# Kernel optimization log

Hardware: AMD Instinct MI355X
Metric: run time of the kernel (lower is better)

## Reference

```python
import jax, jax.numpy as jnp
import numpy as np

N_NODES = 100000


def gcn_conv(x, edge_index, W, b, num_nodes):
    """PyG GCNConv: y = D^{-1/2} (A + I) D^{-1/2} (x W) + b.

    edge_index[0] = source (row), edge_index[1] = target (col);
    messages flow source -> target with symmetric normalization.
    """
    # add self loops
    loop = jnp.arange(num_nodes, dtype=edge_index.dtype)
    row = jnp.concatenate([edge_index[0], loop])  # [E+N]
    col = jnp.concatenate([edge_index[1], loop])  # [E+N]

    xw = x @ W  # [N, F_out] -- tiny GEMM, done before gather

    # degree of target nodes (incl. self loops)
    ones = jnp.ones(col.shape[0], dtype=x.dtype)
    deg = jax.ops.segment_sum(ones, col, num_segments=num_nodes)  # [N]
    dis = jax.lax.rsqrt(jnp.maximum(deg, 1e-12))
    dis = jnp.where(deg > 0, dis, 0.0)

    norm = dis[row] * dis[col]  # [E+N]
    msg = xw[row] * norm[:, None]  # gather + scale, [E+N, F_out]
    out = jax.ops.segment_sum(msg, col, num_segments=num_nodes)  # scatter-add
    return out + b


def setup_inputs() -> dict:
    key = jax.random.key(0)
    k1, k2, k3, k4 = jax.random.split(key, 4)
    num_attr, hidden, num_classes = 128, 16, 8
    n_edges = 3200000
    x = jax.random.normal(k1, (N_NODES, num_attr), dtype=jnp.float32)
    edge_index = jax.random.randint(k2, (2, n_edges), 0, N_NODES, dtype=jnp.int64)
    W1 = jax.random.normal(k3, (num_attr, hidden), dtype=jnp.float32) / np.sqrt(num_attr)
    b1 = jnp.zeros((hidden,), dtype=jnp.float32)
    W2 = jax.random.normal(k4, (hidden, num_classes), dtype=jnp.float32) / np.sqrt(hidden)
    b2 = jnp.zeros((num_classes,), dtype=jnp.float32)
    return {"x": x, "edge_index": edge_index, "W1": W1, "b1": b1, "W2": W2, "b2": b2}


def reference(x, edge_index, W1, b1, W2, b2):
    h = gcn_conv(x, edge_index, W1, b1, N_NODES)
    h = jax.nn.relu(h)
    # dropout is identity in eval mode
    h = gcn_conv(h, edge_index, W2, b2, N_NODES)
    return jax.nn.sigmoid(h)  # [N, num_classes]
```

## Files before the change

### kernel.cpp

```cpp
#include <hip/hip_runtime.h>
#include <math.h>

static constexpr int FI = 128;
static constexpr int FH = 16;
static constexpr int FO = 8;

static constexpr int BIN_SHIFT = 8;
static constexpr int BIN_NODES = 256;
static constexpr int MAX_BINS  = 512;
static constexpr int CAPB      = 8832;
static constexpr int SCHUNK    = 8192;
static constexpr int SThreads  = 512;

__device__ __forceinline__ unsigned short f2bf(float x) {
    unsigned u = __float_as_uint(x);
    u += 0x7FFFu + ((u >> 16) & 1u);
    return (unsigned short)(u >> 16);
}
__device__ __forceinline__ float bflo(unsigned u) { return __uint_as_float(u << 16); }
__device__ __forceinline__ float bfhi(unsigned u) { return __uint_as_float(u & 0xFFFF0000u); }

__global__ void k_initcur(int* __restrict__ binCursor, int nbins) {
    int i = blockIdx.x * 256 + threadIdx.x;
    if (i < nbins) binCursor[i] = i * CAPB;
}

__launch_bounds__(SThreads)
__global__ void k_binscatter(const int* __restrict__ row, const int* __restrict__ col,
                             int* __restrict__ binCursor, unsigned int* __restrict__ binned,
                             int E, int nbins) {
    __shared__ int lcnt[MAX_BINS];
    __shared__ int lsc[MAX_BINS];
    __shared__ int lstart[MAX_BINS];
    __shared__ int lcur[MAX_BINS];
    __shared__ int gbase[MAX_BINS];
    __shared__ unsigned int   staged[SCHUNK];
    __shared__ unsigned short sbin[SCHUNK];
    int t = threadIdx.x;
    int base = blockIdx.x * SCHUNK;
    int end  = base + SCHUNK; if (end > E) end = E;
    int m = end - base;
    if (t < MAX_BINS) lcnt[t] = 0;
    __syncthreads();

    int nv = m >> 2;
    const int4* c4 = (const int4*)(col + base);
    int4 creg[4];
    #pragma unroll
    for (int j = 0; j < 4; ++j) {
        int k = t + j * SThreads;
        if (k < nv) {
            creg[j] = c4[k];
            atomicAdd(&lcnt[creg[j].x >> BIN_SHIFT], 1);
            atomicAdd(&lcnt[creg[j].y >> BIN_SHIFT], 1);
            atomicAdd(&lcnt[creg[j].z >> BIN_SHIFT], 1);
            atomicAdd(&lcnt[creg[j].w >> BIN_SHIFT], 1);
        }
    }
    for (int i = base + (nv << 2) + t; i < end; i += SThreads)
        atomicAdd(&lcnt[col[i] >> BIN_SHIFT], 1);
    __syncthreads();

    int v = 0;
    if (t < MAX_BINS) { v = lcnt[t]; lsc[t] = v; }
    __syncthreads();
    for (int off = 1; off < MAX_BINS; off <<= 1) {
        int x = (t >= off && t < MAX_BINS) ? lsc[t - off] : 0;
        __syncthreads();
        if (t < MAX_BINS) lsc[t] += x;
        __syncthreads();
    }
    if (t < MAX_BINS) {
        int ex = lsc[t] - v;
        lstart[t] = ex;
        lcur[t]   = ex;
        gbase[t]  = v ? atomicAdd(&binCursor[t], v) : 0;
    }
    __syncthreads();

    const int4* r4 = (const int4*)(row + base);
    #pragma unroll
    for (int j = 0; j < 4; ++j) {
        int k = t + j * SThreads;
        if (k < nv) {
            int4 r = r4[k];
            int cc[4] = {creg[j].x, creg[j].y, creg[j].z, creg[j].w};
            int rr[4] = {r.x, r.y, r.z, r.w};
            #pragma unroll
            for (int jj = 0; jj < 4; ++jj) {
                int b = cc[jj] >> BIN_SHIFT;
                int pos = atomicAdd(&lcur[b], 1);
                staged[pos] = (unsigned)rr[jj] | ((unsigned)(cc[jj] & (BIN_NODES - 1)) << 17);
                sbin[pos] = (unsigned short)b;
            }
        }
    }
    for (int i = base + (nv << 2) + t; i < end; i += SThreads) {
        int c = col[i];
        int b = c >> BIN_SHIFT;
        int pos = atomicAdd(&lcur[b], 1);
        staged[pos] = (unsigned)row[i] | ((unsigned)(c & (BIN_NODES - 1)) << 17);
        sbin[pos] = (unsigned short)b;
    }
    __syncthreads();

    for (int i = t; i < m; i += SThreads) {
        int b = sbin[i];
        int g = gbase[b] + (i - lstart[b]);
        if (g < (b + 1) * CAPB) binned[g] = staged[i];
    }
}

__launch_bounds__(256)
__global__ void k_refine_gemm(const int* __restrict__ binCursor, const unsigned int* __restrict__ binned,
                              int* __restrict__ srow, int* __restrict__ starts, int* __restrict__ ends,
                              float* __restrict__ dis, const float* __restrict__ x,
                              const float* __restrict__ W1, unsigned short* __restrict__ xw1s, int N) {
    __shared__ int cnt[BIN_NODES];
    __shared__ int wsum[4];
    __shared__ float sdis[BIN_NODES];
    __shared__ float sw[FI * FH];
    __shared__ float sx[64 * 132];
    int t = threadIdx.x;
    int b = blockIdx.x;
    int s = b * CAPB;
    int m = binCursor[b] - s;
    if (m > CAPB) m = CAPB;
    cnt[t] = 0;
    for (int i = t; i < FI * FH; i += 256) sw[i] = W1[i];
    __syncthreads();

    int mm = m & ~3;
    for (int i0 = t * 4; i0 < mm; i0 += BIN_NODES * 4) {
        uint4 v = *(const uint4*)(binned + s + i0);
        atomicAdd(&cnt[v.x >> 17], 1);
        atomicAdd(&cnt[v.y >> 17], 1);
        atomicAdd(&cnt[v.z >> 17], 1);
        atomicAdd(&cnt[v.w >> 17], 1);
    }
    for (int i = mm + t; i < m; i += BIN_NODES)
        atomicAdd(&cnt[binned[s + i] >> 17], 1);
    __syncthreads();

    int deg = cnt[t];
    int inc = deg;
    #pragma unroll
    for (int d = 1; d < 64; d <<= 1) {
        int u = __shfl_up(inc, d, 64);
        if ((t & 63) >= d) inc += u;
    }
    if ((t & 63) == 63) wsum[t >> 6] = inc;
    __syncthreads();
    if (t < 4) {
        int w = wsum[t];
        #pragma unroll
        for (int d = 1; d < 4; d <<= 1) {
            int u = __shfl_up(w, d, 4);
            if (t >= d) w += u;
        }
        wsum[t] = w;
    }
    __syncthreads();
    int waveoff = (t >= 64) ? wsum[(t >> 6) - 1] : 0;
    int excl = waveoff + inc - deg;

    int n = b * BIN_NODES + t;
    float dv = rsqrtf((float)(deg + 1));
    if (n < N) {
        starts[n] = s + excl;
        ends[n]   = s + excl + deg;
        dis[n]    = dv;
    }
    sdis[t] = dv;
    cnt[t] = excl;
    __syncthreads();

    for (int i0 = t * 4; i0 < mm; i0 += BIN_NODES * 4) {
        uint4 v = *(const uint4*)(binned + s + i0);
        int p0 = atomicAdd(&cnt[v.x >> 17], 1); srow[s + p0] = v.x & 0x1FFFF;
        int p1 = atomicAdd(&cnt[v.y >> 17], 1); srow[s + p1] = v.y & 0x1FFFF;
        int p2 = atomicAdd(&cnt[v.z >> 17], 1); srow[s + p2] = v.z & 0x1FFFF;
        int p3 = atomicAdd(&cnt[v.w >> 17], 1); srow[s + p3] = v.w & 0x1FFFF;
    }
    for (int i = mm + t; i < m; i += BIN_NODES) {
        unsigned v = binned[s + i];
        int p = atomicAdd(&cnt[v >> 17], 1);
        srow[s + p] = v & 0x1FFFF;
    }

    int nl = t >> 2;
    int f  = (t & 3) * 4;
    for (int c = 0; c < 4; ++c) {
        __syncthreads();
        int rbase = b * BIN_NODES + c * 64;
        int rows = N - rbase;
        rows = rows < 0 ? 0 : (rows > 64 ? 64 : rows);
        const float4* xg = (const float4*)(x + (size_t)rbase * FI);
        for (int i = t; i < rows * 32; i += 256) {
            int r = i >> 5, cc = i & 31;
            float4 vv = xg[(size_t)r * 32 + cc];
            float* dst = &sx[r * 132 + cc * 4];
            dst[0] = vv.x; dst[1] = vv.y; dst[2] = vv.z; dst[3] = vv.w;
        }
        __syncthreads();
        int nn = rbase + nl;
        if (nn < N) {
            float a0 = 0.f, a1 = 0.f, a2 = 0.f, a3 = 0.f;
            #pragma unroll 4
            for (int k = 0; k < FI; k++) {
                float xv = sx[nl * 132 + k];
                const float* wr = &sw[k * FH + f];
                a0 = fmaf(xv, wr[0], a0);
                a1 = fmaf(xv, wr[1], a1);
                a2 = fmaf(xv, wr[2], a2);
                a3 = fmaf(xv, wr[3], a3);
            }
            float dn = sdis[c * 64 + nl];
            unsigned w0 = (unsigned)f2bf(a0 * dn) | ((unsigned)f2bf(a1 * dn) << 16);
            unsigned w1 = (unsigned)f2bf(a2 * dn) | ((unsigned)f2bf(a3 * dn) << 16);
            *(uint2*)(xw1s + (size_t)nn * FH + f) = make_uint2(w0, w1);
        }
    }
}

__launch_bounds__(256)
__global__ void k_agg1(const int* __restrict__ starts, const int* __restrict__ ends,
                       const int* __restrict__ srow, const float* __restrict__ dis,
                       const unsigned short* __restrict__ xw1s, const float* __restrict__ W2,
                       const float* __restrict__ b1, unsigned short* __restrict__ xw2s, int N) {
    __shared__ float sw[FH * FO];
    __shared__ float sb[FH];
    int t = threadIdx.x;
    if (t < FH * FO) sw[t] = W2[t];
    if (t < FH) sb[t] = b1[t];
    __syncthreads();

    int n = blockIdx.x * 128 + (t >> 1);
    int h = t & 1;
    if (n >= N) return;
    float dn = dis[n];
    int s = starts[n], e = ends[n];
    const uint4* xq = (const uint4*)xw1s;

    uint4 sp = xq[(size_t)n * 2 + h];
    float acc[8];
    acc[0]=bflo(sp.x); acc[1]=bfhi(sp.x); acc[2]=bflo(sp.y); acc[3]=bfhi(sp.y);
    acc[4]=bflo(sp.z); acc[5]=bfhi(sp.z); acc[6]=bflo(sp.w); acc[7]=bfhi(sp.w);

    int i = s;
    for (; i + 8 <= e; i += 8) {
        int rr[8];
        #pragma unroll
        for (int j = 0; j < 8; ++j) rr[j] = srow[i + j];
        uint4 pk[8];
        #pragma unroll
        for (int j = 0; j < 8; ++j) pk[j] = xq[(size_t)rr[j] * 2 + h];
        #pragma unroll
        for (int j = 0; j < 8; ++j) {
            acc[0]+=bflo(pk[j].x); acc[1]+=bfhi(pk[j].x);
            acc[2]+=bflo(pk[j].y); acc[3]+=bfhi(pk[j].y);
            acc[4]+=bflo(pk[j].z); acc[5]+=bfhi(pk[j].z);
            acc[6]+=bflo(pk[j].w); acc[7]+=bfhi(pk[j].w);
        }
    }
    for (; i < e; ++i) {
        uint4 p = xq[(size_t)srow[i] * 2 + h];
        acc[0]+=bflo(p.x); acc[1]+=bfhi(p.x);
        acc[2]+=bflo(p.y); acc[3]+=bfhi(p.y);
        acc[4]+=bflo(p.z); acc[5]+=bfhi(p.z);
        acc[6]+=bflo(p.w); acc[7]+=bfhi(p.w);
    }

    float hv[8];
    #pragma unroll
    for (int k = 0; k < 8; ++k) {
        float v = fmaf(dn, acc[k], sb[h * 8 + k]);
        hv[k] = v > 0.f ? v : 0.f;
    }
    float po[FO];
    #pragma unroll
    for (int o = 0; o < FO; ++o) {
        float a = 0.f;
        #pragma unroll
        for (int k = 0; k < 8; ++k) a = fmaf(hv[k], sw[(h * 8 + k) * FO + o], a);
        po[o] = a;
    }
    #pragma unroll
    for (int o = 0; o < FO; ++o) po[o] += __shfl_xor(po[o], 1, 64);
    int o0 = h * 4;
    unsigned w0 = (unsigned)f2bf(po[o0 + 0] * dn) | ((unsigned)f2bf(po[o0 + 1] * dn) << 16);
    unsigned w1 = (unsigned)f2bf(po[o0 + 2] * dn) | ((unsigned)f2bf(po[o0 + 3] * dn) << 16);
    *(uint2*)(xw2s + (size_t)n * FO + o0) = make_uint2(w0, w1);
}

__launch_bounds__(256)
__global__ void k_agg2(const int* __restrict__ starts, const int* __restrict__ ends,
                       const int* __restrict__ srow, const float* __restrict__ dis,
                       const unsigned short* __restrict__ xw2s, const float* __restrict__ b2,
                       float* __restrict__ out, int N) {
    int t = threadIdx.x;
    int n = blockIdx.x * 128 + (t >> 1);
    int h = t & 1;
    if (n >= N) return;
    float dn = dis[n];
    int s = starts[n], e = ends[n];
    const uint2* xq = (const uint2*)xw2s;

    uint2 sp = xq[(size_t)n * 2 + h];
    float acc[4];
    acc[0]=bflo(sp.x); acc[1]=bfhi(sp.x); acc[2]=bflo(sp.y); acc[3]=bfhi(sp.y);

    int i = s;
    for (; i + 8 <= e; i += 8) {
        int rr[8];
        #pragma unroll
        for (int j = 0; j < 8; ++j) rr[j] = srow[i + j];
        uint2 pk[8];
        #pragma unroll
        for (int j = 0; j < 8; ++j) pk[j] = xq[(size_t)rr[j] * 2 + h];
        #pragma unroll
        for (int j = 0; j < 8; ++j) {
            acc[0]+=bflo(pk[j].x); acc[1]+=bfhi(pk[j].x);
            acc[2]+=bflo(pk[j].y); acc[3]+=bfhi(pk[j].y);
        }
    }
    for (; i < e; ++i) {
        uint2 p = xq[(size_t)srow[i] * 2 + h];
        acc[0]+=bflo(p.x); acc[1]+=bfhi(p.x);
        acc[2]+=bflo(p.y); acc[3]+=bfhi(p.y);
    }

    int f0 = h * 4;
    float r[4];
    #pragma unroll
    for (int k = 0; k < 4; ++k) {
        float v = fmaf(dn, acc[k], b2[f0 + k]);
        r[k] = 1.f / (1.f + __expf(-v));
    }
    *(float4*)(out + (size_t)n * FO + f0) = make_float4(r[0], r[1], r[2], r[3]);
}

extern "C" void kernel_launch(void* const* d_in, const int* in_sizes, int n_in,
                              void* d_out, int out_size, void* d_ws, size_t ws_size,
                              hipStream_t stream) {
    const float* x  = (const float*)d_in[0];
    const int*   ei = (const int*)d_in[1];
    const float* W1 = (const float*)d_in[2];
    const float* b1 = (const float*)d_in[3];
    const float* W2 = (const float*)d_in[4];
    const float* b2 = (const float*)d_in[5];

    const int N = in_sizes[0] / FI;
    const int E = in_sizes[1] / 2;
    const int* row = ei;
    const int* col = ei + E;
    const int nbins = (N + BIN_NODES - 1) >> BIN_SHIFT;

    const size_t NP = 100352;
    const size_t BINSZ = (size_t)nbins * CAPB;
    float* base = (float*)d_ws;
    int*   starts    = (int*)base;
    int*   ends      = (int*)(base + NP);
    float* dis       = base + 2 * NP;
    int*   binCursor = (int*)(base + 3 * NP);
    unsigned int* binned = (unsigned int*)(base + 3 * NP + 1024);
    int*   srow      = (int*)(base + 3 * NP + 1024 + BINSZ);
    unsigned short* xw1s = (unsigned short*)(base + 3 * NP + 1024 + 2 * BINSZ);
    unsigned short* xw2s = (unsigned short*)(base + 3 * NP + 1024 + 2 * BINSZ + NP * 8);
    float* out = (float*)d_out;

    size_t needed = (3 * NP + 1024 + 2 * BINSZ + NP * 12) * 4;
    if (ws_size < needed) return;

    k_initcur    <<<(nbins + 255) / 256, 256,             0, stream>>>(binCursor, nbins);
    k_binscatter <<<(E + SCHUNK - 1) / SCHUNK, SThreads,  0, stream>>>(row, col, binCursor, binned, E, nbins);
    k_refine_gemm<<<nbins, BIN_NODES,                     0, stream>>>(binCursor, binned, srow, starts, ends, dis, x, W1, xw1s, N);
    k_agg1       <<<(2 * N + 255) / 256, 256,             0, stream>>>(starts, ends, srow, dis, xw1s, W2, b1, xw2s, N);
    k_agg2       <<<(2 * N + 255) / 256, 256,             0, stream>>>(starts, ends, srow, dis, xw2s, b2, out, N);
}
```

Baseline: 125.9 us.

## Split refine and GEMM kernels, stage bins in LDS, use wave-shuffle scan

The fused refine+GEMM kernel is split into a counting-sort refine kernel and a standalone GEMM kernel launched over all nodes with 64 nodes per block. The refine step now stages the bin in LDS and records per-edge local ranks, so the second pass avoids rereading global memory and redoing atomics. The binscatter prefix scan is rewritten as a wave-shuffle scan, cutting the number of barriers. The cursor init kernel is replaced by a memset with relative offsets. This adds a kernel launch and a reread of dis from global memory, but the GEMM gets a full grid of parallelism rather than one block per bin.

```diff
diff --git a/kernel.cpp b/kernel.cpp
--- a/kernel.cpp
+++ b/kernel.cpp
@@ -20,27 +20,22 @@
 __device__ __forceinline__ float bflo(unsigned u) { return __uint_as_float(u << 16); }
 __device__ __forceinline__ float bfhi(unsigned u) { return __uint_as_float(u & 0xFFFF0000u); }
 
-__global__ void k_initcur(int* __restrict__ binCursor, int nbins) {
-    int i = blockIdx.x * 256 + threadIdx.x;
-    if (i < nbins) binCursor[i] = i * CAPB;
-}
-
 __launch_bounds__(SThreads)
 __global__ void k_binscatter(const int* __restrict__ row, const int* __restrict__ col,
                              int* __restrict__ binCursor, unsigned int* __restrict__ binned,
                              int E, int nbins) {
     __shared__ int lcnt[MAX_BINS];
-    __shared__ int lsc[MAX_BINS];
     __shared__ int lstart[MAX_BINS];
     __shared__ int lcur[MAX_BINS];
     __shared__ int gbase[MAX_BINS];
+    __shared__ int wsum[8];
     __shared__ unsigned int   staged[SCHUNK];
     __shared__ unsigned short sbin[SCHUNK];
     int t = threadIdx.x;
     int base = blockIdx.x * SCHUNK;
     int end  = base + SCHUNK; if (end > E) end = E;
     int m = end - base;
-    if (t < MAX_BINS) lcnt[t] = 0;
+    lcnt[t] = 0;
     __syncthreads();
 
     int nv = m >> 2;
@@ -61,17 +56,28 @@
         atomicAdd(&lcnt[col[i] >> BIN_SHIFT], 1);
     __syncthreads();
 
-    int v = 0;
-    if (t < MAX_BINS) { v = lcnt[t]; lsc[t] = v; }
-    __syncthreads();
-    for (int off = 1; off < MAX_BINS; off <<= 1) {
-        int x = (t >= off && t < MAX_BINS) ? lsc[t - off] : 0;
-        __syncthreads();
-        if (t < MAX_BINS) lsc[t] += x;
-        __syncthreads();
-    }
-    if (t < MAX_BINS) {
-        int ex = lsc[t] - v;
+    int v = lcnt[t];
+    int inc = v;
+    #pragma unroll
+    for (int d = 1; d < 64; d <<= 1) {
+        int u = __shfl_up(inc, d, 64);
+        if ((t & 63) >= d) inc += u;
+    }
+    if ((t & 63) == 63) wsum[t >> 6] = inc;
+    __syncthreads();
+    if (t < 8) {
+        int w = wsum[t];
+        #pragma unroll
+        for (int d = 1; d < 8; d <<= 1) {
+            int u = __shfl_up(w, d, 8);
+            if (t >= d) w += u;
+        }
+        wsum[t] = w;
+    }
+    __syncthreads();
+    {
+        int waveoff = (t >= 64) ? wsum[(t >> 6) - 1] : 0;
+        int ex = waveoff + inc - v;
         lstart[t] = ex;
         lcur[t]   = ex;
         gbase[t]  = v ? atomicAdd(&binCursor[t], v) : 0;
@@ -106,40 +112,41 @@
 
     for (int i = t; i < m; i += SThreads) {
         int b = sbin[i];
-        int g = gbase[b] + (i - lstart[b]);
-        if (g < (b + 1) * CAPB) binned[g] = staged[i];
-    }
-}
-
-__launch_bounds__(256)
-__global__ void k_refine_gemm(const int* __restrict__ binCursor, const unsigned int* __restrict__ binned,
-                              int* __restrict__ srow, int* __restrict__ starts, int* __restrict__ ends,
-                              float* __restrict__ dis, const float* __restrict__ x,
-                              const float* __restrict__ W1, unsigned short* __restrict__ xw1s, int N) {
+        int off = gbase[b] + (i - lstart[b]);
+        if (off < CAPB) binned[b * CAPB + off] = staged[i];
+    }
+}
+
+__launch_bounds__(BIN_NODES)
+__global__ void k_refine(const int* __restrict__ binCursor, const unsigned int* __restrict__ binned,
+                         int* __restrict__ srow, int* __restrict__ starts, int* __restrict__ ends,
+                         float* __restrict__ dis, int N) {
+    __shared__ unsigned int  stage[CAPB];
+    __shared__ unsigned char arr[CAPB];
     __shared__ int cnt[BIN_NODES];
     __shared__ int wsum[4];
-    __shared__ float sdis[BIN_NODES];
-    __shared__ float sw[FI * FH];
-    __shared__ float sx[64 * 132];
     int t = threadIdx.x;
     int b = blockIdx.x;
     int s = b * CAPB;
-    int m = binCursor[b] - s;
+    int m = binCursor[b];
     if (m > CAPB) m = CAPB;
     cnt[t] = 0;
-    for (int i = t; i < FI * FH; i += 256) sw[i] = W1[i];
     __syncthreads();
 
     int mm = m & ~3;
     for (int i0 = t * 4; i0 < mm; i0 += BIN_NODES * 4) {
         uint4 v = *(const uint4*)(binned + s + i0);
-        atomicAdd(&cnt[v.x >> 17], 1);
-        atomicAdd(&cnt[v.y >> 17], 1);
-        atomicAdd(&cnt[v.z >> 17], 1);
-        atomicAdd(&cnt[v.w >> 17], 1);
-    }
-    for (int i = mm + t; i < m; i += BIN_NODES)
-        atomicAdd(&cnt[binned[s + i] >> 17], 1);
+        *(uint4*)&stage[i0] = v;
+        arr[i0 + 0] = (unsigned char)atomicAdd(&cnt[v.x >> 17], 1);
+        arr[i0 + 1] = (unsigned char)atomicAdd(&cnt[v.y >> 17], 1);
+        arr[i0 + 2] = (unsigned char)atomicAdd(&cnt[v.z >> 17], 1);
+        arr[i0 + 3] = (unsigned char)atomicAdd(&cnt[v.w >> 17], 1);
+    }
+    for (int i = mm + t; i < m; i += BIN_NODES) {
+        unsigned v = binned[s + i];
+        stage[i] = v;
+        arr[i] = (unsigned char)atomicAdd(&cnt[v >> 17], 1);
+    }
     __syncthreads();
 
     int deg = cnt[t];
@@ -165,62 +172,63 @@
     int excl = waveoff + inc - deg;
 
     int n = b * BIN_NODES + t;
-    float dv = rsqrtf((float)(deg + 1));
     if (n < N) {
         starts[n] = s + excl;
         ends[n]   = s + excl + deg;
-        dis[n]    = dv;
-    }
-    sdis[t] = dv;
+        dis[n]    = rsqrtf((float)(deg + 1));
+    }
     cnt[t] = excl;
     __syncthreads();
 
     for (int i0 = t * 4; i0 < mm; i0 += BIN_NODES * 4) {
-        uint4 v = *(const uint4*)(binned + s + i0);
-        int p0 = atomicAdd(&cnt[v.x >> 17], 1); srow[s + p0] = v.x & 0x1FFFF;
-        int p1 = atomicAdd(&cnt[v.y >> 17], 1); srow[s + p1] = v.y & 0x1FFFF;
-        int p2 = atomicAdd(&cnt[v.z >> 17], 1); srow[s + p2] = v.z & 0x1FFFF;
-        int p3 = atomicAdd(&cnt[v.w >> 17], 1); srow[s + p3] = v.w & 0x1FFFF;
+        uint4 v = *(uint4*)&stage[i0];
+        srow[s + cnt[v.x >> 17] + arr[i0 + 0]] = v.x & 0x1FFFF;
+        srow[s + cnt[v.y >> 17] + arr[i0 + 1]] = v.y & 0x1FFFF;
+        srow[s + cnt[v.z >> 17] + arr[i0 + 2]] = v.z & 0x1FFFF;
+        srow[s + cnt[v.w >> 17] + arr[i0 + 3]] = v.w & 0x1FFFF;
     }
     for (int i = mm + t; i < m; i += BIN_NODES) {
-        unsigned v = binned[s + i];
-        int p = atomicAdd(&cnt[v >> 17], 1);
-        srow[s + p] = v & 0x1FFFF;
-    }
+        unsigned v = stage[i];
+        srow[s + cnt[v >> 17] + arr[i]] = v & 0x1FFFF;
+    }
+}
+
+__launch_bounds__(256)
+__global__ void k_gemm1(const float* __restrict__ x, const float* __restrict__ W,
+                        const float* __restrict__ dis, unsigned short* __restrict__ xw1s,
+                        int N) {
+    __shared__ float sw[FI * FH];
+    int t = threadIdx.x;
+    for (int i = t; i < FI * FH; i += 256) sw[i] = W[i];
+    __syncthreads();
 
     int nl = t >> 2;
     int f  = (t & 3) * 4;
-    for (int c = 0; c < 4; ++c) {
-        __syncthreads();
-        int rbase = b * BIN_NODES + c * 64;
-        int rows = N - rbase;
-        rows = rows < 0 ? 0 : (rows > 64 ? 64 : rows);
-        const float4* xg = (const float4*)(x + (size_t)rbase * FI);
-        for (int i = t; i < rows * 32; i += 256) {
-            int r = i >> 5, cc = i & 31;
-            float4 vv = xg[(size_t)r * 32 + cc];
-            float* dst = &sx[r * 132 + cc * 4];
-            dst[0] = vv.x; dst[1] = vv.y; dst[2] = vv.z; dst[3] = vv.w;
-        }
-        __syncthreads();
-        int nn = rbase + nl;
-        if (nn < N) {
-            float a0 = 0.f, a1 = 0.f, a2 = 0.f, a3 = 0.f;
-            #pragma unroll 4
-            for (int k = 0; k < FI; k++) {
-                float xv = sx[nl * 132 + k];
-                const float* wr = &sw[k * FH + f];
-                a0 = fmaf(xv, wr[0], a0);
-                a1 = fmaf(xv, wr[1], a1);
-                a2 = fmaf(xv, wr[2], a2);
-                a3 = fmaf(xv, wr[3], a3);
-            }
-            float dn = sdis[c * 64 + nl];
-            unsigned w0 = (unsigned)f2bf(a0 * dn) | ((unsigned)f2bf(a1 * dn) << 16);
-            unsigned w1 = (unsigned)f2bf(a2 * dn) | ((unsigned)f2bf(a3 * dn) << 16);
-            *(uint2*)(xw1s + (size_t)nn * FH + f) = make_uint2(w0, w1);
-        }
-    }
+    int n  = blockIdx.x * 64 + nl;
+    if (n >= N) return;
+
+    const float4* xr = (const float4*)(x + (size_t)n * FI);
+    float a0 = 0.f, a1 = 0.f, a2 = 0.f, a3 = 0.f;
+    #pragma unroll 8
+    for (int kq = 0; kq < FI / 4; ++kq) {
+        float4 xv = xr[kq];
+        float4 w0 = *(const float4*)&sw[(kq * 4 + 0) * FH + f];
+        float4 w1 = *(const float4*)&sw[(kq * 4 + 1) * FH + f];
+        float4 w2 = *(const float4*)&sw[(kq * 4 + 2) * FH + f];
+        float4 w3 = *(const float4*)&sw[(kq * 4 + 3) * FH + f];
+        a0 = fmaf(xv.x, w0.x, a0); a1 = fmaf(xv.x, w0.y, a1);
+        a2 = fmaf(xv.x, w0.z, a2); a3 = fmaf(xv.x, w0.w, a3);
+        a0 = fmaf(xv.y, w1.x, a0); a1 = fmaf(xv.y, w1.y, a1);
+        a2 = fmaf(xv.y, w1.z, a2); a3 = fmaf(xv.y, w1.w, a3);
+        a0 = fmaf(xv.z, w2.x, a0); a1 = fmaf(xv.z, w2.y, a1);
+        a2 = fmaf(xv.z, w2.z, a2); a3 = fmaf(xv.z, w2.w, a3);
+        a0 = fmaf(xv.w, w3.x, a0); a1 = fmaf(xv.w, w3.y, a1);
+        a2 = fmaf(xv.w, w3.z, a2); a3 = fmaf(xv.w, w3.w, a3);
+    }
+    float dn = dis[n];
+    unsigned w0 = (unsigned)f2bf(a0 * dn) | ((unsigned)f2bf(a1 * dn) << 16);
+    unsigned w1 = (unsigned)f2bf(a2 * dn) | ((unsigned)f2bf(a3 * dn) << 16);
+    *(uint2*)(xw1s + (size_t)n * FH + f) = make_uint2(w0, w1);
 }
 
 __launch_bounds__(256)
@@ -372,9 +380,10 @@
     size_t needed = (3 * NP + 1024 + 2 * BINSZ + NP * 12) * 4;
     if (ws_size < needed) return;
 
-    k_initcur    <<<(nbins + 255) / 256, 256,             0, stream>>>(binCursor, nbins);
-    k_binscatter <<<(E + SCHUNK - 1) / SCHUNK, SThreads,  0, stream>>>(row, col, binCursor, binned, E, nbins);
-    k_refine_gemm<<<nbins, BIN_NODES,                     0, stream>>>(binCursor, binned, srow, starts, ends, dis, x, W1, xw1s, N);
-    k_agg1       <<<(2 * N + 255) / 256, 256,             0, stream>>>(starts, ends, srow, dis, xw1s, W2, b1, xw2s, N);
-    k_agg2       <<<(2 * N + 255) / 256, 256,             0, stream>>>(starts, ends, srow, dis, xw2s, b2, out, N);
-}
+    hipMemsetAsync(binCursor, 0, (size_t)nbins * sizeof(int), stream);
+    k_binscatter<<<(E + SCHUNK - 1) / SCHUNK, SThreads,  0, stream>>>(row, col, binCursor, binned, E, nbins);
+    k_refine    <<<nbins, BIN_NODES,                     0, stream>>>(binCursor, binned, srow, starts, ends, dis, N);
+    k_gemm1     <<<(N + 63) / 64, 256,                   0, stream>>>(x, W1, dis, xw1s, N);
+    k_agg1      <<<(2 * N + 255) / 256, 256,             0, stream>>>(starts, ends, srow, dis, xw1s, W2, b1, xw2s, N);
+    k_agg2      <<<(2 * N + 255) / 256, 256,             0, stream>>>(starts, ends, srow, dis, xw2s, b2, out, N);
+}
```

Result: faster. 122.2 us (-2.9%).
